# Optimization experiments

Hardware: AMD Instinct MI355X
Metric: run time of the kernel (lower is better)

The kernel has to match this reference:

```python
import jax, jax.numpy as jnp
import numpy as np

N_NODES = 20000
IN_FEAT = 128
CONV_OUT = 32
N_EDGES = 640000
FC1_OUT = 128


def setup_inputs() -> dict:
    key = jax.random.key(0)
    ks = jax.random.split(key, 8)
    x = jax.random.normal(ks[0], (N_NODES, IN_FEAT), dtype=jnp.float32)
    edge_index = jax.random.randint(ks[1], (2, N_EDGES), 0, N_NODES, dtype=jnp.int64)
    # GCNConv params (PyG: lin weight [in, out] applied as x @ W, plus bias)
    w_conv = jax.random.normal(ks[2], (IN_FEAT, CONV_OUT), dtype=jnp.float32) * (1.0 / np.sqrt(IN_FEAT))
    b_conv = jnp.zeros((CONV_OUT,), dtype=jnp.float32)
    # fc1: Linear(32*N -> 128), torch stores weight as [out, in]
    w_fc1 = jax.random.normal(ks[3], (FC1_OUT, CONV_OUT * N_NODES), dtype=jnp.float32) * (1.0 / np.sqrt(CONV_OUT * N_NODES))
    b_fc1 = jnp.zeros((FC1_OUT,), dtype=jnp.float32)
    # fc2: Linear(128 -> N)
    w_fc2 = jax.random.normal(ks[4], (N_NODES, FC1_OUT), dtype=jnp.float32) * (1.0 / np.sqrt(FC1_OUT))
    b_fc2 = jnp.zeros((N_NODES,), dtype=jnp.float32)
    return {"x": x, "edge_index": edge_index, "w_conv": w_conv, "b_conv": b_conv,
            "w_fc1": w_fc1, "b_fc1": b_fc1, "w_fc2": w_fc2, "b_fc2": b_fc2}


def gcn_conv(x, edge_index, w, b):
    # PyG GCNConv default: add self-loops, symmetric normalization D^-1/2 (A+I) D^-1/2
    n = x.shape[0]
    loop = jnp.arange(n, dtype=edge_index.dtype)
    src = jnp.concatenate([edge_index[0], loop])  # [E+N]
    dst = jnp.concatenate([edge_index[1], loop])
    deg = jax.ops.segment_sum(jnp.ones_like(dst, dtype=x.dtype), dst, num_segments=n)
    dinv = jnp.where(deg > 0, jax.lax.rsqrt(deg), 0.0)
    norm = dinv[src] * dinv[dst]  # [E+N]
    h = x @ w  # [N, out] — transform before propagate
    msg = h[src] * norm[:, None]  # gather
    agg = jax.ops.segment_sum(msg, dst, num_segments=n)  # scatter-add
    return agg + b


def reference(x, edge_index, w_conv, b_conv, w_fc1, b_fc1, w_fc2, b_fc2):
    h1 = jax.nn.relu(gcn_conv(x, edge_index, w_conv, b_conv))  # [N, 32]; dropout inactive (eval)
    flat = h1.reshape(-1, CONV_OUT * N_NODES)  # [1, 32*N]
    h3 = jax.nn.relu(flat @ w_fc1.T + b_fc1)   # [1, 128]
    out = jax.nn.relu(h3 @ w_fc2.T + b_fc2)    # [1, N] q-values
    return out
```

## Files before the change

kernel.cpp:

```cpp
#include <hip/hip_runtime.h>

#define N_NODES 20000
#define IN_FEAT 128
#define CONV_OUT 32
#define N_EDGES 640000
#define FC1_OUT 128


#define GEMM1_BLOCKS 313
#define ZERO_INT4 5001

__global__ __launch_bounds__(256) void k1_gemm_zero(const float* __restrict__ x,
                                                    const float* __restrict__ w,
                                                    float* __restrict__ h,
                                                    int4* __restrict__ zbase) {
    __shared__ float xs[64][132];
    __shared__ float ws[128][32];
    int tid = threadIdx.x;

    if (blockIdx.x >= GEMM1_BLOCKS) {
        int i = (blockIdx.x - GEMM1_BLOCKS) * 256 + tid;
        if (i < ZERO_INT4) zbase[i] = make_int4(0, 0, 0, 0);
        return;
    }
    int n0 = blockIdx.x * 64;

    const float4* w4 = (const float4*)w;
    float4* ws4 = (float4*)ws;
    #pragma unroll
    for (int i = 0; i < 4; ++i) ws4[i * 256 + tid] = w4[i * 256 + tid];

    const float4* x4 = (const float4*)x;
    #pragma unroll
    for (int i = 0; i < 8; ++i) {
        int idx = i * 256 + tid;
        int nl  = idx >> 5;
        int k4  = idx & 31;
        int n   = n0 + nl;
        float4 v = make_float4(0.f, 0.f, 0.f, 0.f);
        if (n < N_NODES) v = x4[(size_t)n * 32 + k4];
        *(float4*)&xs[nl][k4 * 4] = v;
    }
    __syncthreads();

    int c4  = tid & 7;
    int nl0 = tid >> 3;
    const float4* wsrow = (const float4*)ws;
    #pragma unroll
    for (int p = 0; p < 2; ++p) {
        int nl = nl0 + p * 32;
        float4 acc = make_float4(0.f, 0.f, 0.f, 0.f);
        #pragma unroll 8
        for (int k = 0; k < 128; k += 4) {
            float4 xv  = *(const float4*)&xs[nl][k];
            float4 wv0 = wsrow[(k + 0) * 8 + c4];
            float4 wv1 = wsrow[(k + 1) * 8 + c4];
            float4 wv2 = wsrow[(k + 2) * 8 + c4];
            float4 wv3 = wsrow[(k + 3) * 8 + c4];
            acc.x += xv.x * wv0.x + xv.y * wv1.x + xv.z * wv2.x + xv.w * wv3.x;
            acc.y += xv.x * wv0.y + xv.y * wv1.y + xv.z * wv2.y + xv.w * wv3.y;
            acc.z += xv.x * wv0.z + xv.y * wv1.z + xv.z * wv2.z + xv.w * wv3.z;
            acc.w += xv.x * wv0.w + xv.y * wv1.w + xv.z * wv2.w + xv.w * wv3.w;
        }
        int n = n0 + nl;
        if (n < N_NODES) *(float4*)&h[(size_t)n * 32 + c4 * 4] = acc;
    }
}

__global__ __launch_bounds__(256) void k_degscan(const int* __restrict__ ei,
                                                 int* __restrict__ cnt,
                                                 int* __restrict__ r,
                                                 int* __restrict__ done,
                                                 int* __restrict__ startv,
                                                 float* __restrict__ dinv) {
    __shared__ int ld[20480];
    __shared__ int ps[256];
    __shared__ int sticket;
    int tid = threadIdx.x;
    int t = blockIdx.x * 256 + tid;

    int4 d = ((const int4*)(ei + N_EDGES))[t];
    int4 s;
    s.x = atomicAdd(&cnt[d.x], 1);
    s.y = atomicAdd(&cnt[d.y], 1);
    s.z = atomicAdd(&cnt[d.z], 1);
    s.w = atomicAdd(&cnt[d.w], 1);
    ((int4*)r)[t] = s;

    __syncthreads();
    if (tid == 0) {
        __threadfence();
        sticket = atomicAdd(done, 1);
    }
    __syncthreads();
    if (sticket != (int)gridDim.x - 1) return;

    __threadfence();
    const int4* c4 = (const int4*)cnt;
    int4* l4 = (int4*)ld;
    #pragma unroll
    for (int i = 0; i < 20; ++i) {
        int idx = i * 256 + tid;
        l4[idx] = (idx < N_NODES / 4) ? c4[idx] : make_int4(0, 0, 0, 0);
    }
    __syncthreads();
    int base = tid * 80;
    int sum = 0;
    #pragma unroll 8
    for (int i = 0; i < 80; ++i) sum += ld[base + i];
    ps[tid] = sum;
    __syncthreads();
    for (int off = 1; off < 256; off <<= 1) {
        int v = (tid >= off) ? ps[tid - off] : 0;
        __syncthreads();
        ps[tid] += v;
        __syncthreads();
    }
    int run = (tid == 0) ? 0 : ps[tid - 1];
    #pragma unroll 8
    for (int i = 0; i < 80; ++i) {
        int n = base + i;
        int v = ld[n];
        ld[n] = run;
        if (n < N_NODES) dinv[n] = rsqrtf((float)v + 1.0f);
        run += v;
    }
    __syncthreads();
    const int4* l4c = (const int4*)ld;
    int4* s4 = (int4*)startv;
    #pragma unroll
    for (int i = 0; i < 20; ++i) {
        int idx = i * 256 + tid;
        if (idx < N_NODES / 4) s4[idx] = l4c[idx];
    }
    if (tid == 0) startv[N_NODES] = N_EDGES;
}

__global__ __launch_bounds__(256) void k_fill(const int* __restrict__ ei,
                                              const int* __restrict__ startv,
                                              const int* __restrict__ r,
                                              int* __restrict__ csr) {
    int e = blockIdx.x * 256 + threadIdx.x;
    if (e < N_EDGES) {
        int s = ei[e];
        int d = ei[N_EDGES + e];
        csr[startv[d] + r[e]] = s;
    }
}

__global__ __launch_bounds__(256) void k_gather(const int* __restrict__ startv,
                                                const int* __restrict__ csr,
                                                const float* __restrict__ h,
                                                const float* __restrict__ dinv,
                                                const float* __restrict__ bc,
                                                float* __restrict__ flat) {
    int tid  = threadIdx.x;
    int lane = tid & 63;
    int n    = blockIdx.x * 4 + (tid >> 6);
    if (n >= N_NODES) return;
    int es = lane >> 3;
    int f4 = lane & 7;
    const float4* h4 = (const float4*)h;
    float4 acc = make_float4(0.f, 0.f, 0.f, 0.f);
    int p0 = startv[n], p1 = startv[n + 1];
    #pragma unroll 2
    for (int p = p0 + es; p < p1; p += 8) {
        int s = csr[p];
        float ds = dinv[s];
        float4 v = h4[(size_t)s * 8 + f4];
        acc.x += v.x * ds; acc.y += v.y * ds; acc.z += v.z * ds; acc.w += v.w * ds;
    }
    #pragma unroll
    for (int m = 8; m < 64; m <<= 1) {
        acc.x += __shfl_xor(acc.x, m);
        acc.y += __shfl_xor(acc.y, m);
        acc.z += __shfl_xor(acc.z, m);
        acc.w += __shfl_xor(acc.w, m);
    }
    if (lane < 8) {
        float dv = dinv[n];
        float4 self = h4[(size_t)n * 8 + f4];
        float4 b = ((const float4*)bc)[f4];
        float4 r_;
        r_.x = fmaxf((acc.x + dv * self.x) * dv + b.x, 0.f);
        r_.y = fmaxf((acc.y + dv * self.y) * dv + b.y, 0.f);
        r_.z = fmaxf((acc.z + dv * self.z) * dv + b.z, 0.f);
        r_.w = fmaxf((acc.w + dv * self.w) * dv + b.w, 0.f);
        ((float4*)flat)[(size_t)n * 8 + f4] = r_;
    }
}

#define FC1_CH 25
__global__ __launch_bounds__(256) void k_fc1(const float* __restrict__ flat,
                                             const float* __restrict__ w,
                                             float* __restrict__ part) {
    int bid = blockIdx.x;
    int jg = bid & 31;
    int ch = bid >> 5;
    int j0 = jg * 4;
    const float4* f4 = (const float4*)flat;
    const size_t row4 = (size_t)CONV_OUT * N_NODES / 4;
    const float4* w0 = (const float4*)w + (size_t)(j0 + 0) * row4;
    const float4* w1 = (const float4*)w + (size_t)(j0 + 1) * row4;
    const float4* w2 = (const float4*)w + (size_t)(j0 + 2) * row4;
    const float4* w3 = (const float4*)w + (size_t)(j0 + 3) * row4;
    int base = ch * 6400;
    float a0 = 0.f, a1 = 0.f, a2 = 0.f, a3 = 0.f;
    #pragma unroll 5
    for (int it = 0; it < 25; ++it) {
        int k = base + it * 256 + threadIdx.x;
        float4 fv  = f4[k];
        float4 v0  = w0[k];
        float4 v1  = w1[k];
        float4 v2  = w2[k];
        float4 v3  = w3[k];
        a0 += v0.x * fv.x + v0.y * fv.y + v0.z * fv.z + v0.w * fv.w;
        a1 += v1.x * fv.x + v1.y * fv.y + v1.z * fv.z + v1.w * fv.w;
        a2 += v2.x * fv.x + v2.y * fv.y + v2.z * fv.z + v2.w * fv.w;
        a3 += v3.x * fv.x + v3.y * fv.y + v3.z * fv.z + v3.w * fv.w;
    }
    #pragma unroll
    for (int o = 32; o > 0; o >>= 1) {
        a0 += __shfl_down(a0, o);
        a1 += __shfl_down(a1, o);
        a2 += __shfl_down(a2, o);
        a3 += __shfl_down(a3, o);
    }
    __shared__ float red[4][4];
    int wv = threadIdx.x >> 6;
    if ((threadIdx.x & 63) == 0) {
        red[wv][0] = a0; red[wv][1] = a1; red[wv][2] = a2; red[wv][3] = a3;
    }
    __syncthreads();
    if (threadIdx.x < 4) {
        float s = red[0][threadIdx.x] + red[1][threadIdx.x] +
                  red[2][threadIdx.x] + red[3][threadIdx.x];
        part[(size_t)(j0 + threadIdx.x) * FC1_CH + ch] = s;
    }
}

__global__ __launch_bounds__(256) void k_fc2(const float* __restrict__ part,
                                             const float* __restrict__ b1,
                                             const float* __restrict__ w2,
                                             const float* __restrict__ b2,
                                             float* __restrict__ out) {
    __shared__ float h3s[128];
    int tid = threadIdx.x;
    if (tid < 128) {
        const float* p = part + (size_t)tid * FC1_CH;
        float s = 0.f;
        #pragma unroll
        for (int i = 0; i < FC1_CH; ++i) s += p[i];
        h3s[tid] = fmaxf(s + b1[tid], 0.f);
    }
    __syncthreads();
    int i = blockIdx.x * 256 + tid;
    if (i < N_NODES) {
        const float4* wr = (const float4*)(w2 + (size_t)i * FC1_OUT);
        const float4* h4 = (const float4*)h3s;
        float acc = b2[i];
        #pragma unroll
        for (int j = 0; j < 32; ++j) {
            float4 wv = wr[j];
            float4 hv = h4[j];
            acc += wv.x * hv.x + wv.y * hv.y + wv.z * hv.z + wv.w * hv.w;
        }
        out[i] = fmaxf(acc, 0.f);
    }
}

extern "C" void kernel_launch(void* const* d_in, const int* in_sizes, int n_in,
                              void* d_out, int out_size, void* d_ws, size_t ws_size,
                              hipStream_t stream) {
    const float* x      = (const float*)d_in[0];
    const int*   ei     = (const int*)d_in[1];
    const float* w_conv = (const float*)d_in[2];
    const float* b_conv = (const float*)d_in[3];
    const float* w_fc1  = (const float*)d_in[4];
    const float* b_fc1  = (const float*)d_in[5];
    const float* w_fc2  = (const float*)d_in[6];
    const float* b_fc2  = (const float*)d_in[7];
    float* ws = (float*)d_ws;
    int*   cnt    = (int*)ws;
    int*   done   = (int*)(ws + 20000);
    float* part   = ws + 20004;
    int*   startv = (int*)(ws + 23204);
    float* dinv   = ws + 43208;
    int*   r      = (int*)(ws + 63208);
    int*   csr    = (int*)(ws + 703208);
    float* h      = ws + 1343208;
    float* flat   = ws + 1983208;
    float* out    = (float*)d_out;

    k1_gemm_zero<<<GEMM1_BLOCKS + 20, 256, 0, stream>>>(x, w_conv, h, (int4*)d_ws);
    k_degscan<<<N_EDGES / 4 / 256, 256, 0, stream>>>(ei, cnt, r, done, startv, dinv);
    k_fill<<<(N_EDGES + 255) / 256, 256, 0, stream>>>(ei, startv, r, csr);
    k_gather<<<(N_NODES + 3) / 4, 256, 0, stream>>>(startv, csr, h, dinv, b_conv, flat);
    k_fc1<<<32 * FC1_CH, 256, 0, stream>>>(flat, w_fc1, part);
    k_fc2<<<(N_NODES + 255) / 256, 256, 0, stream>>>(part, b_fc1, w_fc2, b_fc2, out);
}
```

Before: 177.4 us.

## Prescale node features by inverse degree and shrink degree-scan shared memory

The per-edge dinv[src] multiply is moved out of the gather loop: a new set of blocks in the CSR fill kernel scales h rows by dinv once per node, so the gather loop only does the dependent index load and feature load. The degree scan's last-block prefix sum is rewritten to process the counts in five 4096-entry segments, cutting static shared memory from ~80KB to ~16KB so more degree-count blocks can be resident per CU. The segmented scan adds more barriers to the serial tail, and h is now modified in place.

After: 181.3 us. 1.02x slower.

```diff
diff --git a/kernel.cpp b/kernel.cpp
--- a/kernel.cpp
+++ b/kernel.cpp
@@ -73,7 +73,7 @@
                                                  int* __restrict__ done,
                                                  int* __restrict__ startv,
                                                  float* __restrict__ dinv) {
-    __shared__ int ld[20480];
+    __shared__ int ld2[4096];
     __shared__ int ps[256];
     __shared__ int sticket;
     int tid = threadIdx.x;
@@ -97,54 +97,71 @@
 
     __threadfence();
     const int4* c4 = (const int4*)cnt;
-    int4* l4 = (int4*)ld;
-    #pragma unroll
-    for (int i = 0; i < 20; ++i) {
-        int idx = i * 256 + tid;
-        l4[idx] = (idx < N_NODES / 4) ? c4[idx] : make_int4(0, 0, 0, 0);
-    }
-    __syncthreads();
-    int base = tid * 80;
-    int sum = 0;
-    #pragma unroll 8
-    for (int i = 0; i < 80; ++i) sum += ld[base + i];
-    ps[tid] = sum;
-    __syncthreads();
-    for (int off = 1; off < 256; off <<= 1) {
-        int v = (tid >= off) ? ps[tid - off] : 0;
+    int4* l4 = (int4*)ld2;
+    int4* s4 = (int4*)startv;
+    int segbase = 0;
+    #pragma unroll 1
+    for (int seg = 0; seg < 5; ++seg) {
+        #pragma unroll
+        for (int i = 0; i < 4; ++i) {
+            int idx4 = seg * 1024 + i * 256 + tid;
+            l4[i * 256 + tid] = (idx4 < N_NODES / 4) ? c4[idx4] : make_int4(0, 0, 0, 0);
+        }
         __syncthreads();
-        ps[tid] += v;
+        int base = tid * 16;
+        int sum = 0;
+        #pragma unroll
+        for (int i = 0; i < 16; ++i) sum += ld2[base + i];
+        ps[tid] = sum;
         __syncthreads();
-    }
-    int run = (tid == 0) ? 0 : ps[tid - 1];
-    #pragma unroll 8
-    for (int i = 0; i < 80; ++i) {
-        int n = base + i;
-        int v = ld[n];
-        ld[n] = run;
-        if (n < N_NODES) dinv[n] = rsqrtf((float)v + 1.0f);
-        run += v;
-    }
-    __syncthreads();
-    const int4* l4c = (const int4*)ld;
-    int4* s4 = (int4*)startv;
-    #pragma unroll
-    for (int i = 0; i < 20; ++i) {
-        int idx = i * 256 + tid;
-        if (idx < N_NODES / 4) s4[idx] = l4c[idx];
+        for (int off = 1; off < 256; off <<= 1) {
+            int v = (tid >= off) ? ps[tid - off] : 0;
+            __syncthreads();
+            ps[tid] += v;
+            __syncthreads();
+        }
+        int segtotal = ps[255];
+        int run = segbase + (tid ? ps[tid - 1] : 0);
+        #pragma unroll
+        for (int i = 0; i < 16; ++i) {
+            int n = seg * 4096 + base + i;
+            int v = ld2[base + i];
+            ld2[base + i] = run;
+            if (n < N_NODES) dinv[n] = rsqrtf((float)v + 1.0f);
+            run += v;
+        }
+        __syncthreads();
+        #pragma unroll
+        for (int i = 0; i < 4; ++i) {
+            int idx4 = seg * 1024 + i * 256 + tid;
+            if (idx4 < N_NODES / 4) s4[idx4] = l4[i * 256 + tid];
+        }
+        segbase += segtotal;
+        __syncthreads();
     }
     if (tid == 0) startv[N_NODES] = N_EDGES;
 }
 
-__global__ __launch_bounds__(256) void k_fill(const int* __restrict__ ei,
-                                              const int* __restrict__ startv,
-                                              const int* __restrict__ r,
-                                              int* __restrict__ csr) {
-    int e = blockIdx.x * 256 + threadIdx.x;
-    if (e < N_EDGES) {
+#define FILL_BLOCKS 2500
+#define SCALE_BLOCKS 625
+__global__ __launch_bounds__(256) void k_fill_scale(const int* __restrict__ ei,
+                                                    const int* __restrict__ startv,
+                                                    const int* __restrict__ r,
+                                                    int* __restrict__ csr,
+                                                    const float* __restrict__ dinv,
+                                                    float* __restrict__ h) {
+    int tid = threadIdx.x;
+    if (blockIdx.x < FILL_BLOCKS) {
+        int e = blockIdx.x * 256 + tid;
         int s = ei[e];
         int d = ei[N_EDGES + e];
         csr[startv[d] + r[e]] = s;
+    } else {
+        int i = (blockIdx.x - FILL_BLOCKS) * 256 + tid;
+        float dv = dinv[i >> 3];
+        float4 v = ((float4*)h)[i];
+        v.x *= dv; v.y *= dv; v.z *= dv; v.w *= dv;
+        ((float4*)h)[i] = v;
     }
 }
 
@@ -166,9 +183,8 @@
     #pragma unroll 2
     for (int p = p0 + es; p < p1; p += 8) {
         int s = csr[p];
-        float ds = dinv[s];
         float4 v = h4[(size_t)s * 8 + f4];
-        acc.x += v.x * ds; acc.y += v.y * ds; acc.z += v.z * ds; acc.w += v.w * ds;
+        acc.x += v.x; acc.y += v.y; acc.z += v.z; acc.w += v.w;
     }
     #pragma unroll
     for (int m = 8; m < 64; m <<= 1) {
@@ -178,14 +194,14 @@
         acc.w += __shfl_xor(acc.w, m);
     }
     if (lane < 8) {
+        float4 self = h4[(size_t)n * 8 + f4];
         float dv = dinv[n];
-        float4 self = h4[(size_t)n * 8 + f4];
         float4 b = ((const float4*)bc)[f4];
         float4 r_;
-        r_.x = fmaxf((acc.x + dv * self.x) * dv + b.x, 0.f);
-        r_.y = fmaxf((acc.y + dv * self.y) * dv + b.y, 0.f);
-        r_.z = fmaxf((acc.z + dv * self.z) * dv + b.z, 0.f);
-        r_.w = fmaxf((acc.w + dv * self.w) * dv + b.w, 0.f);
+        r_.x = fmaxf((acc.x + self.x) * dv + b.x, 0.f);
+        r_.y = fmaxf((acc.y + self.y) * dv + b.y, 0.f);
+        r_.z = fmaxf((acc.z + self.z) * dv + b.z, 0.f);
+        r_.w = fmaxf((acc.w + self.w) * dv + b.w, 0.f);
         ((float4*)flat)[(size_t)n * 8 + f4] = r_;
     }
 }
@@ -294,7 +310,7 @@
 
     k1_gemm_zero<<<GEMM1_BLOCKS + 20, 256, 0, stream>>>(x, w_conv, h, (int4*)d_ws);
     k_degscan<<<N_EDGES / 4 / 256, 256, 0, stream>>>(ei, cnt, r, done, startv, dinv);
-    k_fill<<<(N_EDGES + 255) / 256, 256, 0, stream>>>(ei, startv, r, csr);
+    k_fill_scale<<<FILL_BLOCKS + SCALE_BLOCKS, 256, 0, stream>>>(ei, startv, r, csr, dinv, h);
     k_gather<<<(N_NODES + 3) / 4, 256, 0, stream>>>(startv, csr, h, dinv, b_conv, flat);
     k_fc1<<<32 * FC1_CH, 256, 0, stream>>>(flat, w_fc1, part);
     k_fc2<<<(N_NODES + 255) / 256, 256, 0, stream>>>(part, b_fc1, w_fc2, b_fc2, out);
```
